# Performance work log

Hardware: AMD Instinct MI355X
Metric: run time of the kernel (lower is better)

The kernel has to match this reference:

```python
import jax, jax.numpy as jnp
import numpy as np

N = 4096          # n_neurons
M = 10            # max_memory
T = 10            # max_ticks
B = 1024          # batch
P = N // 2 // 2   # n_pairs = 1024
AD = 64           # attention_dim


def ln(x, g, b, eps=1e-5):
    m = x.mean(-1, keepdims=True)
    v = ((x - m) ** 2).mean(-1, keepdims=True)
    return (x - m) * jax.lax.rsqrt(v + eps) * g + b


def setup_inputs() -> dict:
    key = jax.random.key(0)
    ks = iter(jax.random.split(key, 64))

    def rn(shape, s=0.05):
        return (jax.random.normal(next(ks), shape) * s).astype(jnp.float32)

    d = {}
    d['x'] = jax.random.normal(next(ks), (B, 1, 28, 28), dtype=jnp.float32)
    d['post0'] = jax.random.normal(next(ks), (N, M), dtype=jnp.float32)
    d['pre0'] = jax.random.normal(next(ks), (N, M), dtype=jnp.float32)
    d['pairs'] = jax.random.randint(next(ks), (P, 2), 0, N)
    d['decay'] = jnp.full((P,), 0.1, jnp.float32)
    # image encoder: 784 -> 128 -> 32 -> 4
    d['ie_w1'] = rn((784, 128)); d['ie_b1'] = jnp.zeros(128); d['ie_g1'] = jnp.ones(128); d['ie_be1'] = jnp.zeros(128)
    d['ie_w2'] = rn((128, 32));  d['ie_b2'] = jnp.zeros(32);  d['ie_g2'] = jnp.ones(32);  d['ie_be2'] = jnp.zeros(32)
    d['ie_w3'] = rn((32, 4));    d['ie_b3'] = jnp.zeros(4)
    # synapse model: (4+N) -> 256 -> N
    d['sy_w1'] = rn((4 + N, 256)); d['sy_b1'] = jnp.zeros(256); d['sy_g'] = jnp.ones(256); d['sy_be'] = jnp.zeros(256)
    d['sy_w2'] = rn((256, N));     d['sy_b2'] = jnp.zeros(N)
    # batched per-neuron models: M -> 128 -> 1
    d['nm_w1'] = rn((N, M, 128)); d['nm_b1'] = jnp.zeros((N, 128))
    d['nm_g'] = jnp.ones((N, 128)); d['nm_be'] = jnp.zeros((N, 128))
    d['nm_w2'] = rn((N, 128));    d['nm_b2'] = jnp.zeros(N)
    # attention projections
    d['key_w'] = rn((4, AD)); d['key_b'] = jnp.zeros(AD)
    d['val_w'] = rn((4, AD)); d['val_b'] = jnp.zeros(AD)
    d['q_w'] = rn((P, AD));   d['q_b'] = jnp.zeros(AD)
    # syncronization reader: (AD+P) -> 512 -> 64 -> 10
    d['rd_w1'] = rn((AD + P, 512)); d['rd_b1'] = jnp.zeros(512); d['rd_g1'] = jnp.ones(512); d['rd_be1'] = jnp.zeros(512)
    d['rd_w2'] = rn((512, 64));     d['rd_b2'] = jnp.zeros(64);  d['rd_g2'] = jnp.ones(64);  d['rd_be2'] = jnp.zeros(64)
    d['rd_w3'] = rn((64, 10));      d['rd_b3'] = jnp.zeros(10)
    return d


def reference(x, post0, pre0, pairs, decay,
              ie_w1, ie_b1, ie_g1, ie_be1, ie_w2, ie_b2, ie_g2, ie_be2, ie_w3, ie_b3,
              sy_w1, sy_b1, sy_g, sy_be, sy_w2, sy_b2,
              nm_w1, nm_b1, nm_g, nm_be, nm_w2, nm_b2,
              key_w, key_b, val_w, val_b, q_w, q_b,
              rd_w1, rd_b1, rd_g1, rd_be1, rd_w2, rd_b2, rd_g2, rd_be2, rd_w3, rd_b3):
    b = x.shape[0]
    fx = x.reshape(b, -1)
    # image encoder
    e = jax.nn.relu(ln(fx @ ie_w1 + ie_b1, ie_g1, ie_be1))
    e = jax.nn.relu(ln(e @ ie_w2 + ie_b2, ie_g2, ie_be2))
    enc = e @ ie_w3 + ie_b3                               # [B,4]
    keys = enc @ key_w + key_b                            # [B,AD]
    values = enc @ val_w + val_b                          # [B,AD]
    post, pre = post0, pre0
    pred = None
    for tick in range(T):
        last_post = jnp.broadcast_to(post[:, -1][None, :], (b, N))
        syn_in = jnp.concatenate([enc, last_post], axis=1)            # [B,4+N]
        h = jax.nn.relu(ln(syn_in @ sy_w1 + sy_b1, sy_g, sy_be))
        new_pre = h @ sy_w2 + sy_b2                                   # [B,N]
        pre = jnp.concatenate([pre[:, 1:], new_pre.mean(0)[:, None]], axis=1)
        # batched per-neuron MLP over history
        h2 = jax.nn.relu(ln(jnp.einsum('nm,nmh->nh', pre, nm_w1) + nm_b1, nm_g, nm_be))
        new_post = jnp.einsum('nh,nh->n', h2, nm_w2) + nm_b2          # [N]
        post = jnp.concatenate([post[:, 1:], new_post[:, None]], axis=1)
        # decayed pair synchronization
        L = min(tick + 1, M)
        Zi = post[pairs[:, 0], M - L:]                                # [P,L]
        Zj = post[pairs[:, 1], M - L:]
        td = jnp.arange(L - 1, -1, -1, dtype=post.dtype)              # [L]
        R = jnp.exp(-decay[:, None] * td[None, :])                    # [P,L]
        sync = jnp.sum(Zi * R * Zj, axis=1) / (jnp.sum(R, axis=1) + 1e-8)  # [P]
        sv = jnp.broadcast_to(sync[None, :], (b, P))                  # [B,P]
        q = sv @ q_w + q_b                                            # [B,AD]
        scores = jnp.sum(q * keys, axis=-1, keepdims=True) / jnp.sqrt(jnp.float32(AD))
        aw = jax.nn.softmax(scores, axis=-1)                          # [B,1] -> ones
        att = aw * values                                             # [B,AD]
        comb = jnp.concatenate([att, sv], axis=-1)                    # [B,AD+P]
        r = jax.nn.relu(ln(comb @ rd_w1 + rd_b1, rd_g1, rd_be1))
        r = jax.nn.relu(ln(r @ rd_w2 + rd_b2, rd_g2, rd_be2))
        pred = r @ rd_w3 + rd_b3                                      # [B,10]
    return pred
```

## Files before the change

### kernel.cpp

```cpp
#include <hip/hip_runtime.h>

#define N_ 4096
#define M_ 10
#define T_ 10
#define B_ 1024
#define P_ 1024
#define NBLK 256
#define NTHR 512

__device__ __forceinline__ float wave_red_sum(float v) {
#pragma unroll
  for (int m = 32; m >= 1; m >>= 1) v += __shfl_xor(v, m);
  return v;
}

__device__ __forceinline__ float gld(const float* p) {
  return __hip_atomic_load(p, __ATOMIC_RELAXED, __HIP_MEMORY_SCOPE_AGENT);
}
__device__ __forceinline__ void gst(float* p, float v) {
  __hip_atomic_store(p, v, __ATOMIC_RELAXED, __HIP_MEMORY_SCOPE_AGENT);
}
__device__ __forceinline__ unsigned ld_u(unsigned* p) {
  return __hip_atomic_load(p, __ATOMIC_RELAXED, __HIP_MEMORY_SCOPE_AGENT);
}

__device__ __forceinline__ void drain_sync() {
  asm volatile("s_waitcnt vmcnt(0)" ::: "memory");
  __syncthreads();
}
__device__ __forceinline__ void signal(unsigned* slot, unsigned val) {
  if (threadIdx.x == 0)
    __hip_atomic_store(slot, val, __ATOMIC_RELAXED, __HIP_MEMORY_SCOPE_AGENT);
}
__device__ __forceinline__ void wait_set(unsigned* slots, int n, unsigned target) {
  if (threadIdx.x < 64) {
    int lane = threadIdx.x;
    bool ok;
    do {
      ok = true;
      for (int i = lane; i < n; i += 64) ok &= (ld_u(&slots[i]) >= target);
      ok = __all(ok);
      if (!ok) __builtin_amdgcn_s_sleep(1);
    } while (!ok);
  }
  __syncthreads();
}
__device__ __forceinline__ void wait_mod8(unsigned* slots, int s, unsigned target) {
  if (threadIdx.x < 64) {
    int lane = threadIdx.x;
    bool ok;
    do {
      ok = (lane < 32) ? (ld_u(&slots[s + 8 * lane]) >= target) : true;
      ok = __all(ok);
      if (!ok) __builtin_amdgcn_s_sleep(1);
    } while (!ok);
  }
  __syncthreads();
}

__global__ void k_init(unsigned* __restrict__ bar) {
  if (threadIdx.x < 1024)
    __hip_atomic_store(bar + threadIdx.x, 0u, __ATOMIC_RELAXED, __HIP_MEMORY_SCOPE_AGENT);
}

struct MArgs {
  const float *x, *post0, *pre0;
  const int* pairs;
  const float* decay;
  const float *iew1, *ieb1, *ieg1, *iebe1, *iew2, *ieb2, *ieg2, *iebe2, *iew3, *ieb3;
  const float *syw1, *syb1, *syg, *sybe, *syw2, *syb2;
  const float *nw1, *nb1, *ng, *nbe, *nw2, *nb2;
  const float *vw, *vb;
  const float *rdw1, *rdb1, *rdg1, *rdbe1, *rdw2, *rdb2, *rdg2, *rdbe2, *rdw3, *rdb3;
  float *pc, *pc2, *enc_g, *hbar, *postG, *scp;
  float* out;
  unsigned* bar;
};

__global__ __launch_bounds__(NTHR)
void k_mega(MArgs a) {
  const int g = blockIdx.x, tid = threadIdx.x;
  const int lane = tid & 63;
  const int n0 = g * 16, b0e = g * 4;

  __shared__ float s_w1[16 * M_ * 128];
  __shared__ float s_syw1[16 * 256];
  __shared__ float s_w4[4 * 256];
  __shared__ float s_syw2[256 * 16];
  __shared__ float reg1[4096];
  __shared__ float reg2[1024];
  __shared__ float s_mbrb[2048];
  __shared__ float s_values[4][64];
  __shared__ float s_post[16][M_];
  __shared__ float s_pre[16][M_];
  __shared__ float s_pl[16];
  __shared__ float s_hbar[256];
  __shared__ float s_cval[256];
  __shared__ float s_tmp[2][256];
  __shared__ float s_stats[20];

  unsigned* slotA = a.bar;
  unsigned* slotR = a.bar + 256;
  unsigned* slotC = a.bar + 320;

  {
    const float4* src = (const float4*)(a.nw1 + n0 * M_ * 128);
    float4* dst = (float4*)s_w1;
    for (int i = tid; i < 16 * M_ * 128 / 4; i += NTHR) dst[i] = src[i];
    const float4* s2 = (const float4*)(a.syw1 + (4 + n0) * 256);
    float4* d2 = (float4*)s_syw1;
    for (int i = tid; i < 16 * 256 / 4; i += NTHR) d2[i] = s2[i];
    const float4* s3 = (const float4*)a.syw1;
    float4* d3 = (float4*)s_w4;
    for (int i = tid; i < 1024 / 4; i += NTHR) d3[i] = s3[i];
    for (int i = tid; i < 256 * 4; i += NTHR) {
      int k = i >> 2, part = i & 3;
      *(float4*)&s_syw2[k * 16 + part * 4] =
          *(const float4*)&a.syw2[k * N_ + n0 + part * 4];
    }
    if (tid < 160) {
      int r = tid / 10, m = tid - r * 10;
      s_post[r][m] = a.post0[(n0 + r) * M_ + m];
      s_pre[r][m]  = a.pre0[(n0 + r) * M_ + m];
    }
    for (int i = tid; i < 4 * 784; i += NTHR) reg1[i] = a.x[b0e * 784 + i];
  }
  __syncthreads();
  if (tid < 16) s_pl[tid] = s_post[tid][M_ - 1];

  {
    int r = tid >> 7, j = tid & 127;
    float u = a.ieb1[j];
    const float* fxr = reg1 + r * 784;
    for (int k = 0; k < 784; ++k) u += fxr[k] * a.iew1[k * 128 + j];
    float s = wave_red_sum(u), sq = wave_red_sum(u * u);
    int w = tid >> 6;
    if (lane == 0) { s_tmp[0][w] = s; s_tmp[1][w] = sq; }
    __syncthreads();
    float S = s_tmp[0][r * 2] + s_tmp[0][r * 2 + 1];
    float S2 = s_tmp[1][r * 2] + s_tmp[1][r * 2 + 1];
    float mm = S * (1.f / 128.f), vv = S2 * (1.f / 128.f) - mm * mm;
    reg2[r * 128 + j] = fmaxf((u - mm) * rsqrtf(vv + 1e-5f) * a.ieg1[j] + a.iebe1[j], 0.f);
  }
  __syncthreads();
  if (tid < 128) {
    int r = tid >> 5, jj = tid & 31;
    float u = a.ieb2[jj];
    for (int k = 0; k < 128; ++k) u += reg2[r * 128 + k] * a.iew2[k * 32 + jj];
    float ss = u, sq = u * u;
#pragma unroll
    for (int m = 16; m >= 1; m >>= 1) { ss += __shfl_xor(ss, m, 32); sq += __shfl_xor(sq, m, 32); }
    float mm = ss * (1.f / 32.f), vv = sq * (1.f / 32.f) - mm * mm;
    reg2[512 + r * 32 + jj] = fmaxf((u - mm) * rsqrtf(vv + 1e-5f) * a.ieg2[jj] + a.iebe2[jj], 0.f);
  }
  __syncthreads();
  if (tid < 16) {
    int r = tid >> 2, o = tid & 3;
    float u = a.ieb3[o];
    for (int k = 0; k < 32; ++k) u += reg2[512 + r * 32 + k] * a.iew3[k * 4 + o];
    reg2[640 + r * 4 + o] = u;
    gst(&a.enc_g[(b0e + r) * 4 + o], u);
  }
  __syncthreads();
  if (tid < 256) {
    int r = tid >> 6, v = tid & 63;
    float u = a.vb[v];
#pragma unroll
    for (int o = 0; o < 4; ++o) u += reg2[640 + r * 4 + o] * a.vw[o * 64 + v];
    s_values[r][v] = u;
  }
  __syncthreads();
  {
    int j = tid & 255, half = tid >> 8;
    float acc = 0.f;
#pragma unroll
    for (int r = 0; r < 8; ++r) {
      int n = half * 8 + r;
      acc += s_pl[n] * s_syw1[n * 256 + j];
    }
    s_tmp[half][j] = acc;
  }
  __syncthreads();
  if (tid < 256) gst(&a.pc[g * 256 + tid], s_tmp[0][tid] + s_tmp[1][tid]);
  drain_sync();
  signal(&slotA[g], 1u);

  {
    float q[14];
    if (tid < 256) {
      float wv[4] = {s_w4[tid], s_w4[256 + tid], s_w4[512 + tid], s_w4[768 + tid]};
      int idx = 0;
#pragma unroll
      for (int o = 0; o < 4; ++o) q[idx++] = wv[o];
#pragma unroll
      for (int o = 0; o < 4; ++o)
#pragma unroll
        for (int p = 0; p <= o; ++p) q[idx++] = wv[o] * wv[p];
    } else {
#pragma unroll
      for (int i = 0; i < 14; ++i) q[i] = 0.f;
    }
#pragma unroll
    for (int i = 0; i < 14; ++i) q[i] = wave_red_sum(q[i]);
    int w = tid >> 6;
    if (lane == 0) {
#pragma unroll
      for (int i = 0; i < 14; ++i) s_tmp[1][w * 16 + i] = q[i];
    }
    __syncthreads();
    if (tid < 14) {
      float S = 0.f;
#pragma unroll
      for (int w2 = 0; w2 < 8; ++w2) S += s_tmp[1][w2 * 16 + tid];
      s_stats[6 + tid] = S * (1.f / 256.f);
    }
  }
  __syncthreads();

  for (int t = 0; t < T_; ++t) {
    if (g < 8) {
      wait_mod8(slotA, g, (unsigned)(t + 1));
      int j = tid & 255, half = tid >> 8;
      float acc = 0.f;
#pragma unroll
      for (int i = 0; i < 16; ++i) {
        int r = g + 8 * (half * 16 + i);
        acc += gld(&a.pc[r * 256 + j]);
      }
      s_tmp[half][j] = acc;
      __syncthreads();
      if (tid < 256) gst(&a.pc2[g * 256 + tid], s_tmp[0][tid] + s_tmp[1][tid]);
      drain_sync();
      signal(&slotR[g], (unsigned)(t + 1));
    }
    wait_set(slotR, 8, (unsigned)(t + 1));
    if (t == 0) {
      for (int i = tid; i < 4096; i += NTHR) {
        int b = i >> 2, o = i & 3;
        reg1[o * 1024 + b] = gld(&a.enc_g[i]);
      }
    }
    {
      int j = tid & 255, half = tid >> 8;
      float cp = 0.f;
#pragma unroll
      for (int s = 0; s < 4; ++s) cp += gld(&a.pc2[(half * 4 + s) * 256 + j]);
      s_tmp[half][j] = cp;
    }
    __syncthreads();
    {
      float cv = 0.f;
      if (tid < 256) {
        cv = a.syb1[tid] + s_tmp[0][tid] + s_tmp[1][tid];
        s_cval[tid] = cv;
      }
      float p[6];
      if (tid < 256) {
        p[0] = cv; p[1] = cv * cv;
        p[2] = cv * s_w4[tid]; p[3] = cv * s_w4[256 + tid];
        p[4] = cv * s_w4[512 + tid]; p[5] = cv * s_w4[768 + tid];
      } else {
#pragma unroll
        for (int i = 0; i < 6; ++i) p[i] = 0.f;
      }
      __syncthreads();
#pragma unroll
      for (int i = 0; i < 6; ++i) p[i] = wave_red_sum(p[i]);
      int w = tid >> 6;
      if (lane == 0) {
#pragma unroll
        for (int i = 0; i < 6; ++i) s_tmp[0][w * 8 + i] = p[i];
      }
      __syncthreads();
      if (tid < 6) {
        float S = 0.f;
#pragma unroll
        for (int w2 = 0; w2 < 8; ++w2) S += s_tmp[0][w2 * 8 + tid];
        s_stats[tid] = S * (1.f / 256.f);
      }
      __syncthreads();
    }
    {
#pragma unroll
      for (int h2 = 0; h2 < 2; ++h2) {
        int b = h2 * 512 + tid;
        float e0 = reg1[b], e1v = reg1[1024 + b], e2v = reg1[2048 + b], e3v = reg1[3072 + b];
        float m = s_stats[0] + e0 * s_stats[6] + e1v * s_stats[7] + e2v * s_stats[8] + e3v * s_stats[9];
        float eu2 = s_stats[1] + 2.f * (e0 * s_stats[2] + e1v * s_stats[3] + e2v * s_stats[4] + e3v * s_stats[5]);
        float qf = e0 * e0 * s_stats[10]
                 + 2.f * e1v * e0 * s_stats[11] + e1v * e1v * s_stats[12]
                 + 2.f * e2v * e0 * s_stats[13] + 2.f * e2v * e1v * s_stats[14] + e2v * e2v * s_stats[15]
                 + 2.f * e3v * e0 * s_stats[16] + 2.f * e3v * e1v * s_stats[17]
                 + 2.f * e3v * e2v * s_stats[18] + e3v * e3v * s_stats[19];
        eu2 += qf;
        s_mbrb[b] = m;
        s_mbrb[1024 + b] = rsqrtf(eu2 - m * m + 1e-5f);
      }
      __syncthreads();
    }
    {
      float cj = s_cval[g];
      float w0 = s_w4[g], w1v = s_w4[256 + g], w2v = s_w4[512 + g], w3v = s_w4[768 + g];
      float gj = a.syg[g], bj = a.sybe[g];
      float acc = 0.f;
#pragma unroll
      for (int h2 = 0; h2 < 2; ++h2) {
        int b = h2 * 512 + tid;
        float e0 = reg1[b], e1v = reg1[1024 + b], e2v = reg1[2048 + b], e3v = reg1[3072 + b];
        float u = cj + e0 * w0 + e1v * w1v + e2v * w2v + e3v * w3v;
        float y = (u - s_mbrb[b]) * s_mbrb[1024 + b] * gj + bj;
        acc += fmaxf(y, 0.f);
      }
      acc = wave_red_sum(acc);
      int w = tid >> 6;
      if (lane == 0) s_tmp[0][w] = acc;
      __syncthreads();
      if (tid == 0) {
        float S = 0.f;
#pragma unroll
        for (int w2 = 0; w2 < 8; ++w2) S += s_tmp[0][w2];
        gst(&a.hbar[g], S * (1.f / 1024.f));
      }
    }
    drain_sync();
    signal(&slotC[g], (unsigned)(t + 1));
    wait_set(slotC, 256, (unsigned)(t + 1));
    if (tid < 256) s_hbar[tid] = gld(&a.hbar[tid]);
    __syncthreads();
    {
      int nl = tid & 15, kq = tid >> 4;
      float u = 0.f;
#pragma unroll
      for (int kk = 0; kk < 8; ++kk) {
        int k = kq * 8 + kk;
        u += s_hbar[k] * s_syw2[k * 16 + nl];
      }
      ((float*)s_tmp)[kq * 16 + nl] = u;
    }
    __syncthreads();
    if (tid < 16) {
      float v = a.syb2[n0 + tid];
#pragma unroll
      for (int q2 = 0; q2 < 32; ++q2) v += ((float*)s_tmp)[q2 * 16 + tid];
#pragma unroll
      for (int m = 0; m < M_ - 1; ++m) s_pre[tid][m] = s_pre[tid][m + 1];
      s_pre[tid][M_ - 1] = v;
    }
    __syncthreads();
    {
      int nl = tid >> 5, q = tid & 31;
      int n2 = n0 + nl;
      float pr[M_];
#pragma unroll
      for (int m = 0; m < M_; ++m) pr[m] = s_pre[nl][m];
      float u[4];
#pragma unroll
      for (int k = 0; k < 4; ++k) {
        int j = q + 32 * k;
        float uu = a.nb1[n2 * 128 + j];
#pragma unroll
        for (int m = 0; m < M_; ++m) uu += pr[m] * s_w1[(nl * M_ + m) * 128 + j];
        u[k] = uu;
      }
      float s = u[0] + u[1] + u[2] + u[3];
      float sq = u[0] * u[0] + u[1] * u[1] + u[2] * u[2] + u[3] * u[3];
#pragma unroll
      for (int m = 16; m >= 1; m >>= 1) { s += __shfl_xor(s, m, 32); sq += __shfl_xor(sq, m, 32); }
      float mm = s * (1.f / 128.f), vv = sq * (1.f / 128.f) - mm * mm;
      float ri = rsqrtf(vv + 1e-5f);
      float d = 0.f;
#pragma unroll
      for (int k = 0; k < 4; ++k) {
        int j = q + 32 * k;
        float y = fmaxf((u[k] - mm) * ri * a.ng[n2 * 128 + j] + a.nbe[n2 * 128 + j], 0.f);
        d += y * a.nw2[n2 * 128 + j];
      }
#pragma unroll
      for (int m = 16; m >= 1; m >>= 1) d += __shfl_xor(d, m, 32);
      if (q == 0) {
        float npost = d + a.nb2[n2];
#pragma unroll
        for (int m = 0; m < M_ - 1; ++m) s_post[nl][m] = s_post[nl][m + 1];
        s_post[nl][M_ - 1] = npost;
        s_pl[nl] = npost;
      }
    }
    __syncthreads();
    if (t < T_ - 1) {
      int j = tid & 255, half = tid >> 8;
      float acc = 0.f;
#pragma unroll
      for (int r = 0; r < 8; ++r) {
        int n = half * 8 + r;
        acc += s_pl[n] * s_syw1[n * 256 + j];
      }
      s_tmp[half][j] = acc;
      __syncthreads();
      if (tid < 256) gst(&a.pc[g * 256 + tid], s_tmp[0][tid] + s_tmp[1][tid]);
    } else {
      if (tid < 160) {
        int r = tid / 10, m = tid - r * 10;
        gst(&a.postG[(n0 + r) * M_ + m], s_post[r][m]);
      }
    }
    drain_sync();
    signal(&slotA[g], (unsigned)(t + 2));
  }

  if (g < 8) {
    wait_set(slotA, 256, 11u);
    if (tid < 128) {
      int p = g * 128 + tid;
      int i = a.pairs[p * 2], jn = a.pairs[p * 2 + 1];
      float dc = a.decay[p];
      float num = 0.f, den = 0.f;
#pragma unroll
      for (int l = 0; l < M_; ++l) {
        float r = expf(-dc * (float)(M_ - 1 - l));
        num += gld(&a.postG[i * M_ + l]) * r * gld(&a.postG[jn * M_ + l]);
        den += r;
      }
      s_tmp[0][tid] = num / (den + 1e-8f);
    }
    __syncthreads();
    float acc = 0.f;
    for (int i = 0; i < 128; ++i)
      acc += s_tmp[0][i] * a.rdw1[(64 + g * 128 + i) * 512 + tid];
    gst(&a.scp[g * 512 + tid], acc);
    drain_sync();
    signal(&slotR[g], 11u);
  }
  wait_set(slotR, 8, 11u);
  {
    float* r1 = reg1;
    float* p2 = reg1 + 2048;
    float base = a.rdb1[tid];
#pragma unroll
    for (int s = 0; s < 8; ++s) base += gld(&a.scp[s * 512 + tid]);
    float u[4];
#pragma unroll
    for (int r = 0; r < 4; ++r) u[r] = base;
    for (int k = 0; k < 64; ++k) {
      float w = a.rdw1[k * 512 + tid];
#pragma unroll
      for (int r = 0; r < 4; ++r) u[r] += s_values[r][k] * w;
    }
    int wid = tid >> 6;
#pragma unroll
    for (int r = 0; r < 4; ++r) {
      float s = wave_red_sum(u[r]), sq = wave_red_sum(u[r] * u[r]);
      if (lane == 0) { s_tmp[0][r * 8 + wid] = s; s_tmp[1][r * 8 + wid] = sq; }
    }
    __syncthreads();
    float gg = a.rdg1[tid], bb = a.rdbe1[tid];
#pragma unroll
    for (int r = 0; r < 4; ++r) {
      float S = 0.f, S2 = 0.f;
#pragma unroll
      for (int w = 0; w < 8; ++w) { S += s_tmp[0][r * 8 + w]; S2 += s_tmp[1][r * 8 + w]; }
      float m = S * (1.f / 512.f), v = S2 * (1.f / 512.f) - m * m;
      r1[r * 512 + tid] = fmaxf((u[r] - m) * rsqrtf(v + 1e-5f) * gg + bb, 0.f);
    }
    __syncthreads();
    int o = tid & 63, kq = tid >> 6;
    float u2[4] = {0.f, 0.f, 0.f, 0.f};
#pragma unroll
    for (int kk = 0; kk < 64; ++kk) {
      int k = kq * 64 + kk;
      float w = a.rdw2[k * 64 + o];
#pragma unroll
      for (int r = 0; r < 4; ++r) u2[r] += r1[r * 512 + k] * w;
    }
#pragma unroll
    for (int r = 0; r < 4; ++r) p2[(kq * 4 + r) * 64 + o] = u2[r];
    __syncthreads();
    if (tid < 256) {
      int r = tid >> 6, o2 = tid & 63;
      float v = a.rdb2[o2];
#pragma unroll
      for (int q = 0; q < 8; ++q) v += p2[(q * 4 + r) * 64 + o2];
      float s = wave_red_sum(v), sq = wave_red_sum(v * v);
      float m = s * (1.f / 64.f), var = sq * (1.f / 64.f) - m * m;
      reg2[r * 64 + o2] = fmaxf((v - m) * rsqrtf(var + 1e-5f) * a.rdg2[o2] + a.rdbe2[o2], 0.f);
    }
    __syncthreads();
    if (tid < 40) {
      int r = tid / 10, o3 = tid - r * 10;
      float acc = a.rdb3[o3];
#pragma unroll
      for (int k = 0; k < 64; ++k) acc += reg2[r * 64 + k] * a.rdw3[k * 10 + o3];
      a.out[(b0e + r) * 10 + o3] = acc;
    }
  }
}

extern "C" void kernel_launch(void* const* d_in, const int* in_sizes, int n_in,
                              void* d_out, int out_size, void* d_ws, size_t ws_size,
                              hipStream_t stream) {
  MArgs a;
  a.x     = (const float*)d_in[0];
  a.post0 = (const float*)d_in[1];
  a.pre0  = (const float*)d_in[2];
  a.pairs = (const int*)d_in[3];
  a.decay = (const float*)d_in[4];
  a.iew1  = (const float*)d_in[5];
  a.ieb1  = (const float*)d_in[6];
  a.ieg1  = (const float*)d_in[7];
  a.iebe1 = (const float*)d_in[8];
  a.iew2  = (const float*)d_in[9];
  a.ieb2  = (const float*)d_in[10];
  a.ieg2  = (const float*)d_in[11];
  a.iebe2 = (const float*)d_in[12];
  a.iew3  = (const float*)d_in[13];
  a.ieb3  = (const float*)d_in[14];
  a.syw1  = (const float*)d_in[15];
  a.syb1  = (const float*)d_in[16];
  a.syg   = (const float*)d_in[17];
  a.sybe  = (const float*)d_in[18];
  a.syw2  = (const float*)d_in[19];
  a.syb2  = (const float*)d_in[20];
  a.nw1   = (const float*)d_in[21];
  a.nb1   = (const float*)d_in[22];
  a.ng    = (const float*)d_in[23];
  a.nbe   = (const float*)d_in[24];
  a.nw2   = (const float*)d_in[25];
  a.nb2   = (const float*)d_in[26];
  a.vw    = (const float*)d_in[29];
  a.vb    = (const float*)d_in[30];
  a.rdw1  = (const float*)d_in[33];
  a.rdb1  = (const float*)d_in[34];
  a.rdg1  = (const float*)d_in[35];
  a.rdbe1 = (const float*)d_in[36];
  a.rdw2  = (const float*)d_in[37];
  a.rdb2  = (const float*)d_in[38];
  a.rdg2  = (const float*)d_in[39];
  a.rdbe2 = (const float*)d_in[40];
  a.rdw3  = (const float*)d_in[41];
  a.rdb3  = (const float*)d_in[42];
  a.out = (float*)d_out;

  float* ws = (float*)d_ws;
  a.pc    = ws;
  a.pc2   = ws + 65536;
  a.enc_g = ws + 67584;
  a.hbar  = ws + 71680;
  a.postG = ws + 71936;
  a.scp   = ws + 112896;
  a.bar   = (unsigned*)(ws + 117000);

  k_init<<<1, 1024, 0, stream>>>(a.bar);
  k_mega<<<NBLK, NTHR, 0, stream>>>(a);
}
```

Baseline: 198.4 us.

## Move pc computation earlier, split reducer/hbar roles, pad syw2 shared layout

Computes and publishes the per-block pc partial sums before loading the remaining weights and running the image encoder, so the reduction blocks can start sooner. Blocks 0-7 now only do the pc2 reduction. Blocks 8-255 compute the hbar columns, with blocks 8-15 taking two columns each. A new slot barrier guards the encoder outputs, and the s_syw2 shared array is padded to stride 17 to avoid bank conflicts. The changes lengthen the critical path for blocks 8-15 and add an extra barrier, and correctness depends on the slot offsets and wait counts being consistent.

```diff
diff --git a/kernel.cpp b/kernel.cpp
--- a/kernel.cpp
+++ b/kernel.cpp
@@ -86,7 +86,7 @@
   __shared__ float s_w1[16 * M_ * 128];
   __shared__ float s_syw1[16 * 256];
   __shared__ float s_w4[4 * 256];
-  __shared__ float s_syw2[256 * 16];
+  __shared__ float s_syw2[256 * 17];
   __shared__ float reg1[4096];
   __shared__ float reg2[1024];
   __shared__ float s_mbrb[2048];
@@ -102,32 +102,54 @@
   unsigned* slotA = a.bar;
   unsigned* slotR = a.bar + 256;
   unsigned* slotC = a.bar + 320;
+  unsigned* slotE = a.bar + 576;
+
+  {
+    const float4* s2 = (const float4*)(a.syw1 + (4 + n0) * 256);
+    float4* d2 = (float4*)s_syw1;
+    for (int i = tid; i < 16 * 256 / 4; i += NTHR) d2[i] = s2[i];
+    if (tid < 160) {
+      int r = tid / 10, m = tid - r * 10;
+      s_post[r][m] = a.post0[(n0 + r) * M_ + m];
+      s_pre[r][m]  = a.pre0[(n0 + r) * M_ + m];
+    }
+  }
+  __syncthreads();
+  if (tid < 16) s_pl[tid] = s_post[tid][M_ - 1];
+  __syncthreads();
+  {
+    int j = tid & 255, half = tid >> 8;
+    float acc = 0.f;
+#pragma unroll
+    for (int r = 0; r < 8; ++r) {
+      int n = half * 8 + r;
+      acc += s_pl[n] * s_syw1[n * 256 + j];
+    }
+    s_tmp[half][j] = acc;
+  }
+  __syncthreads();
+  if (tid < 256) gst(&a.pc[g * 256 + tid], s_tmp[0][tid] + s_tmp[1][tid]);
+  drain_sync();
+  signal(&slotA[g], 1u);
 
   {
     const float4* src = (const float4*)(a.nw1 + n0 * M_ * 128);
     float4* dst = (float4*)s_w1;
     for (int i = tid; i < 16 * M_ * 128 / 4; i += NTHR) dst[i] = src[i];
-    const float4* s2 = (const float4*)(a.syw1 + (4 + n0) * 256);
-    float4* d2 = (float4*)s_syw1;
-    for (int i = tid; i < 16 * 256 / 4; i += NTHR) d2[i] = s2[i];
     const float4* s3 = (const float4*)a.syw1;
     float4* d3 = (float4*)s_w4;
     for (int i = tid; i < 1024 / 4; i += NTHR) d3[i] = s3[i];
-    for (int i = tid; i < 256 * 4; i += NTHR) {
+    for (int i = tid; i < 1024; i += NTHR) {
       int k = i >> 2, part = i & 3;
-      *(float4*)&s_syw2[k * 16 + part * 4] =
-          *(const float4*)&a.syw2[k * N_ + n0 + part * 4];
-    }
-    if (tid < 160) {
-      int r = tid / 10, m = tid - r * 10;
-      s_post[r][m] = a.post0[(n0 + r) * M_ + m];
-      s_pre[r][m]  = a.pre0[(n0 + r) * M_ + m];
+      float4 v = *(const float4*)&a.syw2[k * N_ + n0 + part * 4];
+      s_syw2[k * 17 + part * 4 + 0] = v.x;
+      s_syw2[k * 17 + part * 4 + 1] = v.y;
+      s_syw2[k * 17 + part * 4 + 2] = v.z;
+      s_syw2[k * 17 + part * 4 + 3] = v.w;
     }
     for (int i = tid; i < 4 * 784; i += NTHR) reg1[i] = a.x[b0e * 784 + i];
   }
   __syncthreads();
-  if (tid < 16) s_pl[tid] = s_post[tid][M_ - 1];
-
   {
     int r = tid >> 7, j = tid & 127;
     float u = a.ieb1[j];
@@ -169,33 +191,20 @@
     for (int o = 0; o < 4; ++o) u += reg2[640 + r * 4 + o] * a.vw[o * 64 + v];
     s_values[r][v] = u;
   }
-  __syncthreads();
-  {
-    int j = tid & 255, half = tid >> 8;
-    float acc = 0.f;
-#pragma unroll
-    for (int r = 0; r < 8; ++r) {
-      int n = half * 8 + r;
-      acc += s_pl[n] * s_syw1[n * 256 + j];
-    }
-    s_tmp[half][j] = acc;
-  }
-  __syncthreads();
-  if (tid < 256) gst(&a.pc[g * 256 + tid], s_tmp[0][tid] + s_tmp[1][tid]);
   drain_sync();
-  signal(&slotA[g], 1u);
-
-  {
+  signal(&slotE[g], 1u);
+
+  if (g >= 8) {
     float q[14];
     if (tid < 256) {
       float wv[4] = {s_w4[tid], s_w4[256 + tid], s_w4[512 + tid], s_w4[768 + tid]};
       int idx = 0;
 #pragma unroll
-      for (int o = 0; o < 4; ++o) q[idx++] = wv[o];
-#pragma unroll
-      for (int o = 0; o < 4; ++o)
-#pragma unroll
-        for (int p = 0; p <= o; ++p) q[idx++] = wv[o] * wv[p];
+    for (int o = 0; o < 4; ++o) q[idx++] = wv[o];
+#pragma unroll
+    for (int o = 0; o < 4; ++o)
+#pragma unroll
+      for (int p = 0; p <= o; ++p) q[idx++] = wv[o] * wv[p];
     } else {
 #pragma unroll
       for (int i = 0; i < 14; ++i) q[i] = 0.f;
@@ -214,8 +223,8 @@
       for (int w2 = 0; w2 < 8; ++w2) S += s_tmp[1][w2 * 16 + tid];
       s_stats[6 + tid] = S * (1.f / 256.f);
     }
-  }
-  __syncthreads();
+    __syncthreads();
+  }
 
   for (int t = 0; t < T_; ++t) {
     if (g < 8) {
@@ -232,99 +241,107 @@
       if (tid < 256) gst(&a.pc2[g * 256 + tid], s_tmp[0][tid] + s_tmp[1][tid]);
       drain_sync();
       signal(&slotR[g], (unsigned)(t + 1));
-    }
-    wait_set(slotR, 8, (unsigned)(t + 1));
-    if (t == 0) {
-      for (int i = tid; i < 4096; i += NTHR) {
-        int b = i >> 2, o = i & 3;
-        reg1[o * 1024 + b] = gld(&a.enc_g[i]);
-      }
-    }
-    {
-      int j = tid & 255, half = tid >> 8;
-      float cp = 0.f;
-#pragma unroll
-      for (int s = 0; s < 4; ++s) cp += gld(&a.pc2[(half * 4 + s) * 256 + j]);
-      s_tmp[half][j] = cp;
-    }
-    __syncthreads();
-    {
-      float cv = 0.f;
-      if (tid < 256) {
-        cv = a.syb1[tid] + s_tmp[0][tid] + s_tmp[1][tid];
-        s_cval[tid] = cv;
-      }
-      float p[6];
-      if (tid < 256) {
-        p[0] = cv; p[1] = cv * cv;
-        p[2] = cv * s_w4[tid]; p[3] = cv * s_w4[256 + tid];
-        p[4] = cv * s_w4[512 + tid]; p[5] = cv * s_w4[768 + tid];
-      } else {
-#pragma unroll
-        for (int i = 0; i < 6; ++i) p[i] = 0.f;
+    } else {
+      wait_set(slotR, 8, (unsigned)(t + 1));
+      {
+        int j = tid & 255, half = tid >> 8;
+        float cp = 0.f;
+#pragma unroll
+        for (int s = 0; s < 4; ++s) cp += gld(&a.pc2[(half * 4 + s) * 256 + j]);
+        s_tmp[half][j] = cp;
       }
       __syncthreads();
-#pragma unroll
-      for (int i = 0; i < 6; ++i) p[i] = wave_red_sum(p[i]);
-      int w = tid >> 6;
-      if (lane == 0) {
-#pragma unroll
-        for (int i = 0; i < 6; ++i) s_tmp[0][w * 8 + i] = p[i];
-      }
-      __syncthreads();
-      if (tid < 6) {
-        float S = 0.f;
-#pragma unroll
-        for (int w2 = 0; w2 < 8; ++w2) S += s_tmp[0][w2 * 8 + tid];
-        s_stats[tid] = S * (1.f / 256.f);
-      }
-      __syncthreads();
-    }
-    {
-#pragma unroll
-      for (int h2 = 0; h2 < 2; ++h2) {
-        int b = h2 * 512 + tid;
-        float e0 = reg1[b], e1v = reg1[1024 + b], e2v = reg1[2048 + b], e3v = reg1[3072 + b];
-        float m = s_stats[0] + e0 * s_stats[6] + e1v * s_stats[7] + e2v * s_stats[8] + e3v * s_stats[9];
-        float eu2 = s_stats[1] + 2.f * (e0 * s_stats[2] + e1v * s_stats[3] + e2v * s_stats[4] + e3v * s_stats[5]);
-        float qf = e0 * e0 * s_stats[10]
-                 + 2.f * e1v * e0 * s_stats[11] + e1v * e1v * s_stats[12]
-                 + 2.f * e2v * e0 * s_stats[13] + 2.f * e2v * e1v * s_stats[14] + e2v * e2v * s_stats[15]
-                 + 2.f * e3v * e0 * s_stats[16] + 2.f * e3v * e1v * s_stats[17]
-                 + 2.f * e3v * e2v * s_stats[18] + e3v * e3v * s_stats[19];
-        eu2 += qf;
-        s_mbrb[b] = m;
-        s_mbrb[1024 + b] = rsqrtf(eu2 - m * m + 1e-5f);
-      }
-      __syncthreads();
-    }
-    {
-      float cj = s_cval[g];
-      float w0 = s_w4[g], w1v = s_w4[256 + g], w2v = s_w4[512 + g], w3v = s_w4[768 + g];
-      float gj = a.syg[g], bj = a.sybe[g];
-      float acc = 0.f;
-#pragma unroll
-      for (int h2 = 0; h2 < 2; ++h2) {
-        int b = h2 * 512 + tid;
-        float e0 = reg1[b], e1v = reg1[1024 + b], e2v = reg1[2048 + b], e3v = reg1[3072 + b];
-        float u = cj + e0 * w0 + e1v * w1v + e2v * w2v + e3v * w3v;
-        float y = (u - s_mbrb[b]) * s_mbrb[1024 + b] * gj + bj;
-        acc += fmaxf(y, 0.f);
-      }
-      acc = wave_red_sum(acc);
-      int w = tid >> 6;
-      if (lane == 0) s_tmp[0][w] = acc;
-      __syncthreads();
-      if (tid == 0) {
-        float S = 0.f;
-#pragma unroll
-        for (int w2 = 0; w2 < 8; ++w2) S += s_tmp[0][w2];
-        gst(&a.hbar[g], S * (1.f / 1024.f));
-      }
-    }
-    drain_sync();
-    signal(&slotC[g], (unsigned)(t + 1));
-    wait_set(slotC, 256, (unsigned)(t + 1));
+      {
+        float cv = 0.f;
+        if (tid < 256) {
+          cv = a.syb1[tid] + s_tmp[0][tid] + s_tmp[1][tid];
+          s_cval[tid] = cv;
+        }
+        float p[6];
+        if (tid < 256) {
+          p[0] = cv; p[1] = cv * cv;
+          p[2] = cv * s_w4[tid]; p[3] = cv * s_w4[256 + tid];
+          p[4] = cv * s_w4[512 + tid]; p[5] = cv * s_w4[768 + tid];
+        } else {
+#pragma unroll
+          for (int i = 0; i < 6; ++i) p[i] = 0.f;
+        }
+        __syncthreads();
+#pragma unroll
+        for (int i = 0; i < 6; ++i) p[i] = wave_red_sum(p[i]);
+        int w = tid >> 6;
+        if (lane == 0) {
+#pragma unroll
+          for (int i = 0; i < 6; ++i) s_tmp[0][w * 8 + i] = p[i];
+        }
+        __syncthreads();
+        if (tid < 6) {
+          float S = 0.f;
+#pragma unroll
+          for (int w2 = 0; w2 < 8; ++w2) S += s_tmp[0][w2 * 8 + tid];
+          s_stats[tid] = S * (1.f / 256.f);
+        }
+        __syncthreads();
+      }
+      if (t == 0) {
+        wait_set(slotE, 256, 1u);
+        for (int i = tid; i < 4096; i += NTHR) {
+          int b = i >> 2, o = i & 3;
+          reg1[o * 1024 + b] = gld(&a.enc_g[i]);
+        }
+        __syncthreads();
+      }
+      {
+#pragma unroll
+        for (int h2 = 0; h2 < 2; ++h2) {
+          int b = h2 * 512 + tid;
+          float e0 = reg1[b], e1v = reg1[1024 + b], e2v = reg1[2048 + b], e3v = reg1[3072 + b];
+          float m = s_stats[0] + e0 * s_stats[6] + e1v * s_stats[7] + e2v * s_stats[8] + e3v * s_stats[9];
+          float eu2 = s_stats[1] + 2.f * (e0 * s_stats[2] + e1v * s_stats[3] + e2v * s_stats[4] + e3v * s_stats[5]);
+          float qf = e0 * e0 * s_stats[10]
+                   + 2.f * e1v * e0 * s_stats[11] + e1v * e1v * s_stats[12]
+                   + 2.f * e2v * e0 * s_stats[13] + 2.f * e2v * e1v * s_stats[14] + e2v * e2v * s_stats[15]
+                   + 2.f * e3v * e0 * s_stats[16] + 2.f * e3v * e1v * s_stats[17]
+                   + 2.f * e3v * e2v * s_stats[18] + e3v * e3v * s_stats[19];
+          eu2 += qf;
+          s_mbrb[b] = m;
+          s_mbrb[1024 + b] = rsqrtf(eu2 - m * m + 1e-5f);
+        }
+        __syncthreads();
+      }
+      {
+        int ncol = (g < 16) ? 2 : 1;
+        for (int c = 0; c < ncol; ++c) {
+          int jj = c ? (g - 8) : g;
+          float cj = s_cval[jj];
+          float w0 = s_w4[jj], w1v = s_w4[256 + jj], w2v = s_w4[512 + jj], w3v = s_w4[768 + jj];
+          float gj = a.syg[jj], bj = a.sybe[jj];
+          float acc = 0.f;
+#pragma unroll
+          for (int h2 = 0; h2 < 2; ++h2) {
+            int b = h2 * 512 + tid;
+            float e0 = reg1[b], e1v = reg1[1024 + b], e2v = reg1[2048 + b], e3v = reg1[3072 + b];
+            float u = cj + e0 * w0 + e1v * w1v + e2v * w2v + e3v * w3v;
+            float y = (u - s_mbrb[b]) * s_mbrb[1024 + b] * gj + bj;
+            acc += fmaxf(y, 0.f);
+          }
+          acc = wave_red_sum(acc);
+          int w = tid >> 6;
+          if (lane == 0) s_tmp[0][w] = acc;
+          __syncthreads();
+          if (tid == 0) {
+            float S = 0.f;
+#pragma unroll
+            for (int w2 = 0; w2 < 8; ++w2) S += s_tmp[0][w2];
+            gst(&a.hbar[jj], S * (1.f / 1024.f));
+          }
+          __syncthreads();
+        }
+      }
+      drain_sync();
+      signal(&slotC[g], (unsigned)(t + 1));
+    }
+    wait_set(slotC + 8, 248, (unsigned)(t + 1));
     if (tid < 256) s_hbar[tid] = gld(&a.hbar[tid]);
     __syncthreads();
     {
@@ -333,7 +350,7 @@
 #pragma unroll
       for (int kk = 0; kk < 8; ++kk) {
         int k = kq * 8 + kk;
-        u += s_hbar[k] * s_syw2[k * 16 + nl];
+        u += s_hbar[k] * s_syw2[k * 17 + nl];
       }
       ((float*)s_tmp)[kq * 16 + nl] = u;
     }
```

New measurement: 197.9 us. About the same (-0.3%).
